# Kernel optimization log

Measured on AMD Instinct MI355X. Metric: run time of the kernel, lower is better.

Reference implementation:

```python
import jax, jax.numpy as jnp
import numpy as np

B, F_IN, HID, H, S = 256, 1024, 1024, 16, 128
TEMP = float((HID // H) ** 0.5)  # 8.0


def setup_inputs() -> dict:
    key = jax.random.key(0)
    ks = jax.random.split(key, 7)
    return {
        "x": jax.random.normal(ks[0], (B, F_IN, S), dtype=jnp.float32),
        "Wq": jax.random.normal(ks[1], (HID, F_IN), dtype=jnp.float32) * (1.0 / np.sqrt(F_IN)),
        "bq": jax.random.normal(ks[2], (HID,), dtype=jnp.float32) * 0.01,
        "Wk": jax.random.normal(ks[3], (HID, F_IN), dtype=jnp.float32) * (1.0 / np.sqrt(F_IN)),
        "bk": jax.random.normal(ks[4], (HID,), dtype=jnp.float32) * 0.01,
        "Wo": jax.random.normal(ks[5], (S,), dtype=jnp.float32) * (1.0 / np.sqrt(S)),
        "bo": jax.random.normal(ks[6], (1,), dtype=jnp.float32) * 0.01,
    }


def _to_heads(t):
    # (B, F, S) -> (B, H, S, F//H), matching reshape(B,H,F/H,S).permute(0,1,3,2)
    b, f, s = t.shape
    return t.reshape(b, H, f // H, s).transpose(0, 1, 3, 2)


def reference(x, Wq, bq, Wk, bk, Wo, bo):
    # 1x1 Conv1d == per-position linear over channel dim
    q = jnp.einsum('bis,hi->bhs', x, Wq) + bq[None, :, None]
    k = jnp.einsum('bis,hi->bhs', x, Wk) + bk[None, :, None]
    qh = _to_heads(q)          # (B,H,S,HID/H)
    kh = _to_heads(k)          # (B,H,S,HID/H)
    vh = _to_heads(x)          # (B,H,S,F_IN/H)  -- v is the raw input, unprojected
    scores = jnp.einsum('bhsd,bhtd->bhst', qh, kh) / TEMP
    attn = jax.nn.softmax(scores, axis=-1)
    out = jnp.einsum('bhst,bhtd->bhsd', attn, vh)   # (B,H,S,F_IN/H)
    # _reshape_from_batches: (B,H,S,dv) -> (B, F_IN, S)
    out = out.transpose(0, 1, 3, 2).reshape(x.shape[0], F_IN, S)
    # map_o: Linear(num_users, 1) over last axis, then squeeze
    score = jnp.einsum('bfs,s->bf', out, Wo) + bo[0]
    return score
```

## Files before the change

kernel.cpp:

```cpp
#include <hip/hip_runtime.h>

#define F 1024
#define S 128
#define H 16
#define D 64
#define CK 64
#define NCHUNK 16

typedef short bf16x8 __attribute__((ext_vector_type(8)));
typedef float f32x4  __attribute__((ext_vector_type(4)));

#define XS_UNITS ((size_t)128 * NCHUNK * 2048)
#define WB_UNITS ((size_t)8 * NCHUNK * 2048)
#define WS_NEED ((XS_UNITS + WB_UNITS) * 16)

#define MAIN_LDS_BYTES (8192 * 16 + 8 * 128 * 4 + 128 * 4)

__device__ __forceinline__ unsigned short f2bf(float f) {
    unsigned u = __float_as_uint(f);
    u += 0x7fffu + ((u >> 16) & 1u);
    return (unsigned short)(u >> 16);
}

__device__ __forceinline__ uint4 pack8(const float* f) {
    uint4 u;
    u.x = (unsigned)f2bf(f[0]) | ((unsigned)f2bf(f[1]) << 16);
    u.y = (unsigned)f2bf(f[2]) | ((unsigned)f2bf(f[3]) << 16);
    u.z = (unsigned)f2bf(f[4]) | ((unsigned)f2bf(f[5]) << 16);
    u.w = (unsigned)f2bf(f[6]) | ((unsigned)f2bf(f[7]) << 16);
    return u;
}

typedef __attribute__((address_space(1))) const unsigned int as1_u32;
typedef __attribute__((address_space(3))) unsigned int as3_u32;

__device__ __forceinline__ void async_cp16(const uint4* g, uint4* l) {
    __builtin_amdgcn_global_load_lds((as1_u32*)g, (as3_u32*)l, 16, 0, 0);
}

__device__ __forceinline__ void bar()   { __builtin_amdgcn_s_barrier(); }
__device__ __forceinline__ void sb0()   { __builtin_amdgcn_sched_barrier(0); }
__device__ __forceinline__ void lgkm0() { asm volatile("s_waitcnt lgkmcnt(0)"); }

template<int N> __device__ __forceinline__ void vmw() {
    asm volatile("s_waitcnt vmcnt(%0)" :: "n"(N));
}

__global__ void prep(const float* __restrict__ x,
                     const float* __restrict__ Wq,
                     const float* __restrict__ Wk,
                     uint4* __restrict__ xs,
                     uint4* __restrict__ wb)
{
    __shared__ float4 t4[64 * 33];
    const int tid = threadIdx.x;
    const int blk = blockIdx.x;
    if (blk < 1024) {
        const int b = blk >> 2;
#pragma unroll 1
        for (int cc = 0; cc < 4; ++cc) {
            const int ch = (blk & 3) * 4 + cc;
            const float4* src = (const float4*)(x + ((size_t)b * F + ch * CK) * S);
            float4 v[8];
#pragma unroll
            for (int j = 0; j < 8; ++j) v[j] = src[tid + j * 256];
            __syncthreads();
#pragma unroll
            for (int j = 0; j < 8; ++j) {
                const int e4 = tid + j * 256;
                t4[(e4 >> 5) * 33 + (e4 & 31)] = v[j];
            }
            __syncthreads();
            const float* tile = (const float*)t4;
            uint4* dst = xs + ((size_t)(b >> 1) * NCHUNK + ch) * 2048 + (b & 1) * 128;
#pragma unroll
            for (int j = 0; j < 4; ++j) {
                const int u  = tid + j * 256;
                const int kc = u >> 7;
                const int s  = u & 127;
                float f[8];
#pragma unroll
                for (int jj = 0; jj < 8; ++jj) f[jj] = tile[(kc * 8 + jj) * 132 + s];
                dst[kc * 256 + s] = pack8(f);
            }
        }
    } else {
        const int blk2 = blk - 1024;
        const int h = blk2 >> 2;
#pragma unroll 1
        for (int cc = 0; cc < 4; ++cc) {
            const int ch = (blk2 & 3) * 4 + cc;
            uint4* dst = wb + ((size_t)(h >> 1) * NCHUNK + ch) * 2048 + (h & 1) * 128;
#pragma unroll
            for (int j = 0; j < 4; ++j) {
                const int u  = tid + j * 256;
                const int kc = u >> 7;
                const int m  = u & 127;
                const float* srcp = (m < 64)
                    ? (Wq + (size_t)(h * D + m) * F + ch * CK + kc * 8)
                    : (Wk + (size_t)(h * D + m - 64) * F + ch * CK + kc * 8);
                float f[8];
                float4 a = ((const float4*)srcp)[0];
                float4 c = ((const float4*)srcp)[1];
                f[0] = a.x; f[1] = a.y; f[2] = a.z; f[3] = a.w;
                f[4] = c.x; f[5] = c.y; f[6] = c.z; f[7] = c.w;
                dst[kc * 256 + m] = pack8(f);
            }
        }
    }
}

__device__ __forceinline__ void read4(const uint4* mat, int base, bf16x8 (&r)[4]) {
    r[0] = *(const bf16x8*)&mat[base];
    r[1] = *(const bf16x8*)&mat[base + 16];
    r[2] = *(const bf16x8*)&mat[base + 32];
    r[3] = *(const bf16x8*)&mat[base + 48];
}

template<int RB>
__device__ __forceinline__ void mfma16(f32x4 (&acc)[8][4], const bf16x8 (&af)[4], const bf16x8 (&br)[4]) {
#pragma unroll
    for (int mt = 0; mt < 4; ++mt)
#pragma unroll
        for (int nt = 0; nt < 4; ++nt)
            acc[RB + mt][nt] = __builtin_amdgcn_mfma_f32_16x16x32_bf16(af[mt], br[nt], acc[RB + mt][nt], 0, 0, 0);
}

template<int HALF>
__device__ __forceinline__ void stage_half(uint4* mat, const uint4* wbase, const uint4* xbase,
                                           int tgt, int wv, int lane) {
    const int bufb = (tgt & 1) * 4096;
    const uint4* g;
    int l;
    if constexpr (HALF == 0)      { g = wbase + (size_t)tgt * 2048;        l = bufb;        }
    else if constexpr (HALF == 1) { g = xbase + (size_t)tgt * 2048;        l = bufb + 2048; }
    else if constexpr (HALF == 2) { g = wbase + (size_t)tgt * 2048 + 1024; l = bufb + 1024; }
    else                          { g = xbase + (size_t)tgt * 2048 + 1024; l = bufb + 3072; }
    async_cp16(g + wv * 128 + lane,      &mat[l + wv * 128]);
    async_cp16(g + wv * 128 + 64 + lane, &mat[l + wv * 128 + 64]);
}

template<int CUR, bool I1, bool I2, int W1, int W2, bool DW2>
__device__ __forceinline__ void ktile(uint4* mat, const uint4* wbase, const uint4* xbase,
                                      int t, int wv, int lane, int wm, int wn, int q, int l15,
                                      f32x4 (&acc)[8][4])
{
    bf16x8 af[4], br[4];
    const int abase = CUR * 4096 + wm * 128 + l15;
    const int bbase = CUR * 4096 + 2048 + wn * 64 + l15;
    const int kq = q * 256;
    read4(mat, abase + kq, af);
    read4(mat, bbase + kq, br);
    if constexpr (I1) stage_half<2>(mat, wbase, xbase, t + 1, wv, lane);
    bar(); lgkm0(); sb0();
    __builtin_amdgcn_s_setprio(1); mfma16<0>(acc, af, br); __builtin_amdgcn_s_setprio(0);
    bar(); sb0();
    read4(mat, abase + kq + 64, af);
    if constexpr (I1) stage_half<3>(mat, wbase, xbase, t + 1, wv, lane);
    bar(); lgkm0(); sb0();
    __builtin_amdgcn_s_setprio(1); mfma16<4>(acc, af, br); __builtin_amdgcn_s_setprio(0);
    vmw<W1>(); bar(); sb0();
    read4(mat, abase + kq + 1024, af);
    read4(mat, bbase + kq + 1024, br);
    if constexpr (I2) stage_half<0>(mat, wbase, xbase, t + 2, wv, lane);
    bar(); lgkm0(); sb0();
    __builtin_amdgcn_s_setprio(1); mfma16<0>(acc, af, br); __builtin_amdgcn_s_setprio(0);
    bar(); sb0();
    read4(mat, abase + kq + 1024 + 64, af);
    if constexpr (I2) stage_half<1>(mat, wbase, xbase, t + 2, wv, lane);
    bar(); lgkm0(); sb0();
    __builtin_amdgcn_s_setprio(1); mfma16<4>(acc, af, br); __builtin_amdgcn_s_setprio(0);
    if constexpr (DW2) { vmw<W2>(); bar(); sb0(); }
}

__launch_bounds__(512, 2)
__global__ void attn_main(const float* __restrict__ x,
                          const uint4* __restrict__ xs,
                          const uint4* __restrict__ wb,
                          const float* __restrict__ bq,
                          const float* __restrict__ bk,
                          const float* __restrict__ Wo,
                          const float* __restrict__ bo,
                          float* __restrict__ out)
{
    extern __shared__ char smraw[];
    uint4* mat   = (uint4*)smraw;
    float* wpart = (float*)(smraw + 8192 * 16);

    const int tid  = threadIdx.x;
    const int lane = tid & 63;
    const int wv   = tid >> 6;
    const int l15  = lane & 15;
    const int q    = lane >> 4;
    const int wm   = wv >> 2;
    const int wn   = wv & 3;

    const int g    = blockIdx.x;
    const int xcd  = g & 7;
    const int slot = g >> 3;
    const int bg   = xcd * 16 + (slot & 15);
    const int hg   = slot >> 4;

    const uint4* wbase = wb + (size_t)hg * NCHUNK * 2048;
    const uint4* xbase = xs + (size_t)bg * NCHUNK * 2048;

    f32x4 acc[8][4];
#pragma unroll
    for (int mi = 0; mi < 8; ++mi)
#pragma unroll
        for (int ni = 0; ni < 4; ++ni) acc[mi][ni] = (f32x4){0.f, 0.f, 0.f, 0.f};

    stage_half<0>(mat, wbase, xbase, 0, wv, lane);
    stage_half<1>(mat, wbase, xbase, 0, wv, lane);
    stage_half<2>(mat, wbase, xbase, 0, wv, lane);
    stage_half<3>(mat, wbase, xbase, 0, wv, lane);
    stage_half<0>(mat, wbase, xbase, 1, wv, lane);
    stage_half<1>(mat, wbase, xbase, 1, wv, lane);
    vmw<8>();
    bar(); sb0();

#pragma unroll 1
    for (int i = 0; i < 7; ++i) {
        ktile<0, true, true, 8, 8, true>(mat, wbase, xbase, 2 * i,     wv, lane, wm, wn, q, l15, acc);
        ktile<1, true, true, 8, 8, true>(mat, wbase, xbase, 2 * i + 1, wv, lane, wm, wn, q, l15, acc);
    }
    ktile<0, true,  false, 8, 4, true >(mat, wbase, xbase, 14, wv, lane, wm, wn, q, l15, acc);
    ktile<1, false, false, 0, 0, false>(mat, wbase, xbase, 15, wv, lane, wm, wn, q, l15, acc);

    __syncthreads();

    {
        unsigned short* m16 = (unsigned short*)mat;
        const int hglob = hg * 2 + wm;
#pragma unroll
        for (int rt = 0; rt < 8; ++rt) {
            const int mh0   = rt * 16 + q * 4;
            const int d0    = mh0 & 63;
            const int kbase = (mh0 < 64) ? 0 : 1024;
            float bias4[4];
#pragma unroll
            for (int rr = 0; rr < 4; ++rr)
                bias4[rr] = (mh0 < 64) ? bq[hglob * D + d0 + rr] : bk[hglob * D + d0 + rr];
#pragma unroll
            for (int ct = 0; ct < 4; ++ct) {
                const int col = wn * 64 + ct * 16 + l15;
                const int bj  = col >> 7;
                const int s   = col & 127;
                const int c   = wm * 2 + bj;
                unsigned long long pv = 0;
#pragma unroll
                for (int rr = 0; rr < 4; ++rr)
                    pv |= (unsigned long long)f2bf(acc[rt][ct][rr] + bias4[rr]) << (16 * rr);
                const int unit = c * 2048 + kbase + s * 8 + ((d0 >> 3) ^ (s & 7));
                *(unsigned long long*)&m16[unit * 8 + (d0 & 7)] = pv;
            }
        }
    }
    __syncthreads();

    const int ce   = ((wv >> 2) << 1) | ((wv >> 1) & 1);
    const int half = wv & 1;
    const int qb = ce * 2048;
    const int kb = ce * 2048 + 1024;
    const int bglob = bg * 2 + (ce & 1);
    const int hglob = hg * 2 + (ce >> 1);

    f32x4 p[4][8];
#pragma unroll
    for (int mt = 0; mt < 4; ++mt)
#pragma unroll
        for (int nt = 0; nt < 8; ++nt) p[mt][nt] = (f32x4){0.f, 0.f, 0.f, 0.f};
#pragma unroll
    for (int ks = 0; ks < 2; ++ks) {
        const int kcq = ks * 4 + q;
        bf16x8 a2[4], b2[8];
#pragma unroll
        for (int mt = 0; mt < 4; ++mt) {
            const int row = half * 64 + mt * 16 + l15;
            a2[mt] = *(const bf16x8*)&mat[qb + row * 8 + (kcq ^ (row & 7))];
        }
#pragma unroll
        for (int nt = 0; nt < 8; ++nt) {
            const int trow = nt * 16 + l15;
            b2[nt] = *(const bf16x8*)&mat[kb + trow * 8 + (kcq ^ (trow & 7))];
        }
#pragma unroll
        for (int mt = 0; mt < 4; ++mt)
#pragma unroll
            for (int nt = 0; nt < 8; ++nt)
                p[mt][nt] = __builtin_amdgcn_mfma_f32_16x16x32_bf16(a2[mt], b2[nt], p[mt][nt], 0, 0, 0);
    }

    float pw[8];
#pragma unroll
    for (int nt = 0; nt < 8; ++nt) pw[nt] = 0.f;
#pragma unroll
    for (int mt = 0; mt < 4; ++mt) {
#pragma unroll
        for (int rr = 0; rr < 4; ++rr) {
            const int srow = half * 64 + mt * 16 + q * 4 + rr;
            float e[8];
            float l = 0.f;
#pragma unroll
            for (int nt = 0; nt < 8; ++nt) {
                e[nt] = __expf(fminf(p[mt][nt][rr] * 0.125f, 80.f));
                l += e[nt];
            }
#pragma unroll
            for (int off = 1; off < 16; off <<= 1) l += __shfl_xor(l, off);
            const float cw = Wo[srow] / l;
#pragma unroll
            for (int nt = 0; nt < 8; ++nt) pw[nt] = fmaf(cw, e[nt], pw[nt]);
        }
    }
#pragma unroll
    for (int nt = 0; nt < 8; ++nt) {
        pw[nt] += __shfl_xor(pw[nt], 16);
        pw[nt] += __shfl_xor(pw[nt], 32);
    }
    if (q == 0) {
#pragma unroll
        for (int nt = 0; nt < 8; ++nt) wpart[wv * 128 + nt * 16 + l15] = pw[nt];
    }
    __syncthreads();

    {
        const int local = half * 64 + lane;
        const int dd    = local >> 1;
        const int part  = local & 1;
        const float* w0 = wpart + 2 * ce * 128;
        const float* w1 = wpart + (2 * ce + 1) * 128;
        const float4* xv = (const float4*)(x + (size_t)bglob * (F * S)
                                             + (size_t)(hglob * D + dd) * S + part * 64);
        float a5 = 0.f;
#pragma unroll
        for (int j = 0; j < 16; ++j) {
            float4 vv = xv[j];
            const int t = part * 64 + j * 4;
            a5 = fmaf(w0[t + 0] + w1[t + 0], vv.x, a5);
            a5 = fmaf(w0[t + 1] + w1[t + 1], vv.y, a5);
            a5 = fmaf(w0[t + 2] + w1[t + 2], vv.z, a5);
            a5 = fmaf(w0[t + 3] + w1[t + 3], vv.w, a5);
        }
        a5 += __shfl_xor(a5, 1);
        if (part == 0) out[(size_t)bglob * F + hglob * D + dd] = a5 + bo[0];
    }
}

struct SmemT {
    uint4 mat[2048];
    float wpart[4][S];
    float wfin[S];
};

__launch_bounds__(256, 4)
__global__ void attn_fallback(const float* __restrict__ x,
                              const float* __restrict__ Wq,
                              const float* __restrict__ bq,
                              const float* __restrict__ Wk,
                              const float* __restrict__ bk,
                              const float* __restrict__ Wo,
                              const float* __restrict__ bo,
                              float* __restrict__ out)
{
    __shared__ SmemT sm;
    const int tid  = threadIdx.x;
    const int lane = tid & 63;
    const int wv   = tid >> 6;
    const int l15  = lane & 15;
    const int q    = lane >> 4;

    const int g    = blockIdx.x;
    const int xcd  = g & 7;
    const int slot = g >> 3;
    const int hg   = slot >> 7;
    const int r0   = slot & 127;
    const int b    = xcd * 32 + (r0 >> 2);
    const int h    = hg * 4 + (r0 & 3);

    const float* xb  = x  + (size_t)b * (F * S);
    const float* wqh = Wq + (size_t)h * D * F;
    const float* wkh = Wk + (size_t)h * D * F;

    const int m0 = (wv & 1) * 64;
    const int n0 = (wv >> 1) * 64;

    f32x4 acc[4][4];
#pragma unroll
    for (int mt = 0; mt < 4; ++mt)
#pragma unroll
        for (int nt = 0; nt < 4; ++nt) acc[mt][nt] = (f32x4){0.f, 0.f, 0.f, 0.f};

    const int mq  = tid >> 2;
    const int kq  = tid & 3;
    const int s0x = (tid & 63) * 2;
    const int iq  = tid >> 6;

    for (int ch = 0; ch < NCHUNK; ++ch) {
        const int c0 = ch * CK;
        __syncthreads();
        {
            const int key = mq & 7;
            float f[16];
            const float4* srcq = (const float4*)(wqh + (size_t)mq * F + (c0 + kq * 16));
#pragma unroll
            for (int j = 0; j < 4; ++j) {
                float4 v = srcq[j];
                f[4*j] = v.x; f[4*j+1] = v.y; f[4*j+2] = v.z; f[4*j+3] = v.w;
            }
            sm.mat[mq * 8 + ((kq * 2    ) ^ key)] = pack8(f);
            sm.mat[mq * 8 + ((kq * 2 + 1) ^ key)] = pack8(f + 8);
            const float4* srck = (const float4*)(wkh + (size_t)mq * F + (c0 + kq * 16));
#pragma unroll
            for (int j = 0; j < 4; ++j) {
                float4 v = srck[j];
                f[4*j] = v.x; f[4*j+1] = v.y; f[4*j+2] = v.z; f[4*j+3] = v.w;
            }
            sm.mat[(64 + mq) * 8 + ((kq * 2    ) ^ key)] = pack8(f);
            sm.mat[(64 + mq) * 8 + ((kq * 2 + 1) ^ key)] = pack8(f + 8);
        }
        {
            const float* src = xb + (size_t)(c0 + iq * 16) * S + s0x;
            float fa[8], fb[8];
#pragma unroll
            for (int grp = 0; grp < 2; ++grp) {
#pragma unroll
                for (int j = 0; j < 8; ++j) {
                    float2 v = *(const float2*)(src + (size_t)(grp * 8 + j) * S);
                    fa[j] = v.x; fb[j] = v.y;
                }
                const int kc = iq * 2 + grp;
                sm.mat[1024 + (s0x    ) * 8 + (kc ^ ((s0x    ) & 7))] = pack8(fa);
                sm.mat[1024 + (s0x + 1) * 8 + (kc ^ ((s0x + 1) & 7))] = pack8(fb);
            }
        }
        __syncthreads();
#pragma unroll
        for (int ks = 0; ks < 2; ++ks) {
            bf16x8 af[4], br[4];
#pragma unroll
            for (int mt = 0; mt < 4; ++mt) {
                const int row = m0 + mt * 16 + l15;
                af[mt] = *(const bf16x8*)&sm.mat[row * 8 + ((ks * 4 + q) ^ (row & 7))];
            }
#pragma unroll
            for (int nt = 0; nt < 4; ++nt) {
                const int row = n0 + nt * 16 + l15;
                br[nt] = *(const bf16x8*)&sm.mat[1024 + row * 8 + ((ks * 4 + q) ^ (row & 7))];
            }
#pragma unroll
            for (int mt = 0; mt < 4; ++mt)
#pragma unroll
                for (int nt = 0; nt < 4; ++nt)
                    acc[mt][nt] = __builtin_amdgcn_mfma_f32_16x16x32_bf16(
                        af[mt], br[nt], acc[mt][nt], 0, 0, 0);
        }
    }

    __syncthreads();
    {
        unsigned short* m16 = (unsigned short*)sm.mat;
#pragma unroll
        for (int mt = 0; mt < 4; ++mt) {
#pragma unroll
            for (int rr = 0; rr < 4; ++rr) {
                const int m = m0 + mt * 16 + q * 4 + rr;
                const int d = m & 63;
                const float bias = (m < 64) ? bq[h * D + d] : bk[h * D + d];
                const int base = (m < 64) ? 0 : 8192;
#pragma unroll
                for (int nt = 0; nt < 4; ++nt) {
                    const int s = n0 + nt * 16 + l15;
                    const float v = acc[mt][nt][rr] + bias;
                    const int unit = s * 8 + (((d >> 3)) ^ (s & 7));
                    m16[base + unit * 8 + (d & 7)] = f2bf(v);
                }
            }
        }
    }
    __syncthreads();

    f32x4 p[2][8];
#pragma unroll
    for (int mt = 0; mt < 2; ++mt)
#pragma unroll
        for (int nt = 0; nt < 8; ++nt) p[mt][nt] = (f32x4){0.f, 0.f, 0.f, 0.f};

#pragma unroll
    for (int ks = 0; ks < 2; ++ks) {
        bf16x8 a2[2], b2[8];
#pragma unroll
        for (int mt = 0; mt < 2; ++mt) {
            const int row = wv * 32 + mt * 16 + l15;
            a2[mt] = *(const bf16x8*)&sm.mat[row * 8 + ((ks * 4 + q) ^ (row & 7))];
        }
#pragma unroll
        for (int nt = 0; nt < 8; ++nt) {
            const int row = nt * 16 + l15;
            b2[nt] = *(const bf16x8*)&sm.mat[1024 + row * 8 + ((ks * 4 + q) ^ (row & 7))];
        }
#pragma unroll
        for (int mt = 0; mt < 2; ++mt)
#pragma unroll
            for (int nt = 0; nt < 8; ++nt)
                p[mt][nt] = __builtin_amdgcn_mfma_f32_16x16x32_bf16(a2[mt], b2[nt], p[mt][nt], 0, 0, 0);
    }

    float pw[8];
#pragma unroll
    for (int nt = 0; nt < 8; ++nt) pw[nt] = 0.f;

#pragma unroll
    for (int mt = 0; mt < 2; ++mt) {
#pragma unroll
        for (int rr = 0; rr < 4; ++rr) {
            const int srow = wv * 32 + mt * 16 + q * 4 + rr;
            float mx = p[mt][0][rr];
#pragma unroll
            for (int nt = 1; nt < 8; ++nt) mx = fmaxf(mx, p[mt][nt][rr]);
#pragma unroll
            for (int off = 1; off < 16; off <<= 1) mx = fmaxf(mx, __shfl_xor(mx, off));
            float e[8];
            float l = 0.f;
#pragma unroll
            for (int nt = 0; nt < 8; ++nt) {
                e[nt] = __expf((p[mt][nt][rr] - mx) * 0.125f);
                l += e[nt];
            }
#pragma unroll
            for (int off = 1; off < 16; off <<= 1) l += __shfl_xor(l, off);
            const float c = Wo[srow] / l;
#pragma unroll
            for (int nt = 0; nt < 8; ++nt) pw[nt] = fmaf(c, e[nt], pw[nt]);
        }
    }
#pragma unroll
    for (int nt = 0; nt < 8; ++nt) {
        pw[nt] += __shfl_xor(pw[nt], 16);
        pw[nt] += __shfl_xor(pw[nt], 32);
    }
    if (q == 0) {
#pragma unroll
        for (int nt = 0; nt < 8; ++nt) sm.wpart[wv][nt * 16 + l15] = pw[nt];
    }
    __syncthreads();
    if (tid < S)
        sm.wfin[tid] = sm.wpart[0][tid] + sm.wpart[1][tid] + sm.wpart[2][tid] + sm.wpart[3][tid];
    __syncthreads();

    {
        const int dd   = tid >> 2;
        const int part = tid & 3;
        const float* xv = xb + (size_t)(h * D + dd) * S + part * 32;
        float a5 = 0.f;
#pragma unroll 8
        for (int t = 0; t < 32; ++t) a5 = fmaf(sm.wfin[part * 32 + t], xv[t], a5);
        a5 += __shfl_xor(a5, 1);
        a5 += __shfl_xor(a5, 2);
        if (part == 0) out[(size_t)b * F + h * D + dd] = a5 + bo[0];
    }
}

extern "C" void kernel_launch(void* const* d_in, const int* in_sizes, int n_in,
                              void* d_out, int out_size, void* d_ws, size_t ws_size,
                              hipStream_t stream) {
    const float* x  = (const float*)d_in[0];
    const float* Wq = (const float*)d_in[1];
    const float* bq = (const float*)d_in[2];
    const float* Wk = (const float*)d_in[3];
    const float* bk = (const float*)d_in[4];
    const float* Wo = (const float*)d_in[5];
    const float* bo = (const float*)d_in[6];
    float* out = (float*)d_out;

    if (ws_size >= WS_NEED) {
        uint4* xsp = (uint4*)d_ws;
        uint4* wbp = (uint4*)((char*)d_ws + XS_UNITS * 16);
        static bool attr_done = false;
        if (!attr_done) {
            (void)hipFuncSetAttribute(reinterpret_cast<const void*>(attn_main),
                                      hipFuncAttributeMaxDynamicSharedMemorySize, MAIN_LDS_BYTES);
            attr_done = true;
        }
        prep<<<dim3(1024 + 64), dim3(256), 0, stream>>>(x, Wq, Wk, xsp, wbp);
        attn_main<<<dim3(1024), dim3(512), MAIN_LDS_BYTES, stream>>>(x, xsp, wbp, bq, bk, Wo, bo, out);
    } else {
        attn_fallback<<<dim3(256 * H), dim3(256), 0, stream>>>(x, Wq, bq, Wk, bk, Wo, bo, out);
    }
}
```

Before: 397.4 us.

## Split prep into finer blocks and read bf16 staged x in final V-reduction

The prep kernel now launches one block per (batch, chunk) and per (head, chunk) instead of looping over four chunks per block. This raises parallelism and drops a barrier per iteration. The final attention-weighted sum in attn_main now reads the pre-converted bf16 copy of x from the workspace rather than the fp32 original, with the loads issued before the softmax so they overlap with it, and a shuffle reduction across 16 lanes. This halves global bytes in the epilogue but uses bf16-rounded V values, which adds a little error, and adds more shuffles.

Result: faster. 353.0 us (-11.2%).

```diff
diff --git a/kernel.cpp b/kernel.cpp
--- a/kernel.cpp
+++ b/kernel.cpp
@@ -55,57 +55,48 @@
     __shared__ float4 t4[64 * 33];
     const int tid = threadIdx.x;
     const int blk = blockIdx.x;
-    if (blk < 1024) {
-        const int b = blk >> 2;
-#pragma unroll 1
-        for (int cc = 0; cc < 4; ++cc) {
-            const int ch = (blk & 3) * 4 + cc;
-            const float4* src = (const float4*)(x + ((size_t)b * F + ch * CK) * S);
-            float4 v[8];
-#pragma unroll
-            for (int j = 0; j < 8; ++j) v[j] = src[tid + j * 256];
-            __syncthreads();
-#pragma unroll
-            for (int j = 0; j < 8; ++j) {
-                const int e4 = tid + j * 256;
-                t4[(e4 >> 5) * 33 + (e4 & 31)] = v[j];
-            }
-            __syncthreads();
-            const float* tile = (const float*)t4;
-            uint4* dst = xs + ((size_t)(b >> 1) * NCHUNK + ch) * 2048 + (b & 1) * 128;
-#pragma unroll
-            for (int j = 0; j < 4; ++j) {
-                const int u  = tid + j * 256;
-                const int kc = u >> 7;
-                const int s  = u & 127;
-                float f[8];
-#pragma unroll
-                for (int jj = 0; jj < 8; ++jj) f[jj] = tile[(kc * 8 + jj) * 132 + s];
-                dst[kc * 256 + s] = pack8(f);
-            }
+    if (blk < 4096) {
+        const int b = blk >> 4, ch = blk & 15;
+        const float4* src = (const float4*)(x + ((size_t)b * F + ch * CK) * S);
+        float4 v[8];
+#pragma unroll
+        for (int j = 0; j < 8; ++j) v[j] = src[tid + j * 256];
+#pragma unroll
+        for (int j = 0; j < 8; ++j) {
+            const int e4 = tid + j * 256;
+            t4[(e4 >> 5) * 33 + (e4 & 31)] = v[j];
+        }
+        __syncthreads();
+        const float* tile = (const float*)t4;
+        uint4* dst = xs + ((size_t)(b >> 1) * NCHUNK + ch) * 2048 + (b & 1) * 128;
+#pragma unroll
+        for (int j = 0; j < 4; ++j) {
+            const int u  = tid + j * 256;
+            const int kc = u >> 7;
+            const int s  = u & 127;
+            float f[8];
+#pragma unroll
+            for (int jj = 0; jj < 8; ++jj) f[jj] = tile[(kc * 8 + jj) * 132 + s];
+            dst[kc * 256 + s] = pack8(f);
         }
     } else {
-        const int blk2 = blk - 1024;
-        const int h = blk2 >> 2;
-#pragma unroll 1
-        for (int cc = 0; cc < 4; ++cc) {
-            const int ch = (blk2 & 3) * 4 + cc;
-            uint4* dst = wb + ((size_t)(h >> 1) * NCHUNK + ch) * 2048 + (h & 1) * 128;
-#pragma unroll
-            for (int j = 0; j < 4; ++j) {
-                const int u  = tid + j * 256;
-                const int kc = u >> 7;
-                const int m  = u & 127;
-                const float* srcp = (m < 64)
-                    ? (Wq + (size_t)(h * D + m) * F + ch * CK + kc * 8)
-                    : (Wk + (size_t)(h * D + m - 64) * F + ch * CK + kc * 8);
-                float f[8];
-                float4 a = ((const float4*)srcp)[0];
-                float4 c = ((const float4*)srcp)[1];
-                f[0] = a.x; f[1] = a.y; f[2] = a.z; f[3] = a.w;
-                f[4] = c.x; f[5] = c.y; f[6] = c.z; f[7] = c.w;
-                dst[kc * 256 + m] = pack8(f);
-            }
+        const int blk2 = blk - 4096;
+        const int h = blk2 >> 4, ch = blk2 & 15;
+        uint4* dst = wb + ((size_t)(h >> 1) * NCHUNK + ch) * 2048 + (h & 1) * 128;
+#pragma unroll
+        for (int j = 0; j < 4; ++j) {
+            const int u  = tid + j * 256;
+            const int kc = u >> 7;
+            const int m  = u & 127;
+            const float* srcp = (m < 64)
+                ? (Wq + (size_t)(h * D + m) * F + ch * CK + kc * 8)
+                : (Wk + (size_t)(h * D + m - 64) * F + ch * CK + kc * 8);
+            float f[8];
+            float4 a = ((const float4*)srcp)[0];
+            float4 c = ((const float4*)srcp)[1];
+            f[0] = a.x; f[1] = a.y; f[2] = a.z; f[3] = a.w;
+            f[4] = c.x; f[5] = c.y; f[6] = c.z; f[7] = c.w;
+            dst[kc * 256 + m] = pack8(f);
         }
     }
 }
@@ -183,6 +174,7 @@
                           const float* __restrict__ bo,
                           float* __restrict__ out)
 {
+    (void)x;
     extern __shared__ char smraw[];
     uint4* mat   = (uint4*)smraw;
     float* wpart = (float*)(smraw + 8192 * 16);
@@ -231,7 +223,7 @@
 
     {
         unsigned short* m16 = (unsigned short*)mat;
-        const int hglob = hg * 2 + wm;
+        const int hglobw = hg * 2 + wm;
 #pragma unroll
         for (int rt = 0; rt < 8; ++rt) {
             const int mh0   = rt * 16 + q * 4;
@@ -240,7 +232,7 @@
             float bias4[4];
 #pragma unroll
             for (int rr = 0; rr < 4; ++rr)
-                bias4[rr] = (mh0 < 64) ? bq[hglob * D + d0 + rr] : bk[hglob * D + d0 + rr];
+                bias4[rr] = (mh0 < 64) ? bq[hglobw * D + d0 + rr] : bk[hglobw * D + d0 + rr];
 #pragma unroll
             for (int ct = 0; ct < 4; ++ct) {
                 const int col = wn * 64 + ct * 16 + l15;
@@ -291,6 +283,14 @@
                 p[mt][nt] = __builtin_amdgcn_mfma_f32_16x16x32_bf16(a2[mt], b2[nt], p[mt][nt], 0, 0, 0);
     }
 
+    const int ell = half * 64 + lane;
+    const int kc5 = ell >> 4;
+    const int sg5 = ell & 15;
+    const uint4* xsrc = xbase + (size_t)hglob * 2048 + kc5 * 256 + (ce & 1) * 128 + sg5 * 8;
+    uint4 xu[8];
+#pragma unroll
+    for (int jj = 0; jj < 8; ++jj) xu[jj] = xsrc[jj];
+
     float pw[8];
 #pragma unroll
     for (int nt = 0; nt < 8; ++nt) pw[nt] = 0.f;
@@ -325,25 +325,31 @@
     __syncthreads();
 
     {
-        const int local = half * 64 + lane;
-        const int dd    = local >> 1;
-        const int part  = local & 1;
         const float* w0 = wpart + 2 * ce * 128;
-        const float* w1 = wpart + (2 * ce + 1) * 128;
-        const float4* xv = (const float4*)(x + (size_t)bglob * (F * S)
-                                             + (size_t)(hglob * D + dd) * S + part * 64);
-        float a5 = 0.f;
-#pragma unroll
-        for (int j = 0; j < 16; ++j) {
-            float4 vv = xv[j];
-            const int t = part * 64 + j * 4;
-            a5 = fmaf(w0[t + 0] + w1[t + 0], vv.x, a5);
-            a5 = fmaf(w0[t + 1] + w1[t + 1], vv.y, a5);
-            a5 = fmaf(w0[t + 2] + w1[t + 2], vv.z, a5);
-            a5 = fmaf(w0[t + 3] + w1[t + 3], vv.w, a5);
-        }
-        a5 += __shfl_xor(a5, 1);
-        if (part == 0) out[(size_t)bglob * F + hglob * D + dd] = a5 + bo[0];
+        const float* w1 = w0 + 128;
+        float acc8[8];
+#pragma unroll
+        for (int e = 0; e < 8; ++e) acc8[e] = 0.f;
+#pragma unroll
+        for (int jj = 0; jj < 8; ++jj) {
+            const int s = sg5 * 8 + jj;
+            const float w = w0[s] + w1[s];
+            const unsigned* du = (const unsigned*)&xu[jj];
+#pragma unroll
+            for (int dw = 0; dw < 4; ++dw) {
+                const unsigned v = du[dw];
+                acc8[dw * 2 + 0] = fmaf(__uint_as_float(v << 16), w, acc8[dw * 2 + 0]);
+                acc8[dw * 2 + 1] = fmaf(__uint_as_float(v & 0xffff0000u), w, acc8[dw * 2 + 1]);
+            }
+        }
+#pragma unroll
+        for (int e = 0; e < 8; ++e) {
+#pragma unroll
+            for (int off = 1; off < 16; off <<= 1)
+                acc8[e] += __shfl_xor(acc8[e], off);
+        }
+        if (sg5 < 8)
+            out[(size_t)bglob * F + hglob * D + kc5 * 8 + sg5] = acc8[sg5] + bo[0];
     }
 }
 
@@ -582,7 +588,7 @@
                                       hipFuncAttributeMaxDynamicSharedMemorySize, MAIN_LDS_BYTES);
             attr_done = true;
         }
-        prep<<<dim3(1024 + 64), dim3(256), 0, stream>>>(x, Wq, Wk, xsp, wbp);
+        prep<<<dim3(4096 + 256), dim3(256), 0, stream>>>(x, Wq, Wk, xsp, wbp);
         attn_main<<<dim3(1024), dim3(512), MAIN_LDS_BYTES, stream>>>(x, xsp, wbp, bq, bk, Wo, bo, out);
     } else {
         attn_fallback<<<dim3(256 * H), dim3(256), 0, stream>>>(x, Wq, bq, Wk, bk, Wo, bo, out);
```
